# Optimization experiments

Hardware: AMD Instinct MI355X
Metric: run time of the kernel (lower is better)

The kernel has to match this reference:

```python
import jax, jax.numpy as jnp
import numpy as np

N_CELLS = 50000
N_GENES = 2000
HIDDEN = 128
HEADS = 4
HEAD_DIM = HIDDEN // HEADS
E_FULL = 800000
E_PRUNED = 400000
LN_EPS = 1e-6
NEG_SLOPE = 0.2


def setup_inputs() -> dict:
    key = jax.random.key(0)
    ks = jax.random.split(key, 20)
    s_in = 1.0 / np.sqrt(N_GENES)
    s_h = 1.0 / np.sqrt(HIDDEN)
    inp = {
        "node_features": jax.random.normal(ks[0], (N_CELLS, N_GENES), jnp.float32),
        "full_edge_index": jax.random.randint(ks[1], (2, E_FULL), 0, N_CELLS, jnp.int64 if jax.config.jax_enable_x64 else jnp.int32),
        "full_edge_weights": jax.random.uniform(ks[2], (E_FULL, 1), jnp.float32),
        "pruned_edge_index": jax.random.randint(ks[3], (2, E_PRUNED), 0, N_CELLS, jnp.int64 if jax.config.jax_enable_x64 else jnp.int32),
        "pruned_edge_weights": jax.random.uniform(ks[4], (E_PRUNED, 1), jnp.float32),
        "alpha": jax.random.uniform(ks[5], (), jnp.float32),
        # input projection
        "ip_w": jax.random.normal(ks[6], (N_GENES, HIDDEN), jnp.float32) * s_in,
        "ip_b": jnp.zeros((HIDDEN,), jnp.float32),
        # GAT full graph
        "gf_wsrc": jax.random.normal(ks[7], (HIDDEN, HIDDEN), jnp.float32) * s_h,
        "gf_wdst": jax.random.normal(ks[8], (HIDDEN, HIDDEN), jnp.float32) * s_h,
        "gf_wedge": jax.random.normal(ks[9], (1, HIDDEN), jnp.float32),
        "gf_attn": jax.random.normal(ks[10], (HEADS, HEAD_DIM), jnp.float32) * (1.0 / np.sqrt(HEAD_DIM)),
        "gf_bias": jnp.zeros((HIDDEN,), jnp.float32),
        # GAT pruned graph
        "gp_wsrc": jax.random.normal(ks[11], (HIDDEN, HIDDEN), jnp.float32) * s_h,
        "gp_wdst": jax.random.normal(ks[12], (HIDDEN, HIDDEN), jnp.float32) * s_h,
        "gp_wedge": jax.random.normal(ks[13], (1, HIDDEN), jnp.float32),
        "gp_attn": jax.random.normal(ks[14], (HEADS, HEAD_DIM), jnp.float32) * (1.0 / np.sqrt(HEAD_DIM)),
        "gp_bias": jnp.zeros((HIDDEN,), jnp.float32),
        # LayerNorm
        "ln_scale": jnp.ones((HIDDEN,), jnp.float32),
        "ln_bias": jnp.zeros((HIDDEN,), jnp.float32),
    }
    return inp


def _gatv2(h, edge_index, edge_w, wsrc, wdst, wedge, attn, bias):
    """GATv2 with edge features: e_ij = a_h . leaky_relu(Ws h_i + Wd h_j + We w_ij),
    segment-softmax over destination nodes, scatter-aggregate Ws h_src, concat heads."""
    n = h.shape[0]
    src, dst = edge_index[0], edge_index[1]
    hs = (h @ wsrc).reshape(n, HEADS, HEAD_DIM)
    hd = (h @ wdst).reshape(n, HEADS, HEAD_DIM)
    ew = (edge_w @ wedge).reshape(-1, HEADS, HEAD_DIM)  # [E,H,D]
    z = jax.nn.leaky_relu(hs[src] + hd[dst] + ew, NEG_SLOPE)  # [E,H,D]
    logits = jnp.einsum('ehd,hd->eh', z, attn)  # [E,H]
    # segment softmax over incoming edges of each dst node
    m = jax.ops.segment_max(logits, dst, num_segments=n)
    m = jnp.where(jnp.isfinite(m), m, 0.0)
    ex = jnp.exp(logits - m[dst])
    denom = jax.ops.segment_sum(ex, dst, num_segments=n)
    att = ex / (denom[dst] + 1e-16)  # [E,H]
    out = jax.ops.segment_sum(att[..., None] * hs[src], dst, num_segments=n)  # [n,H,D]
    return out.reshape(n, HIDDEN) + bias


def _layer_norm(x, scale, bias):
    mu = jnp.mean(x, axis=-1, keepdims=True)
    var = jnp.mean(jnp.square(x - mu), axis=-1, keepdims=True)
    return (x - mu) * jax.lax.rsqrt(var + LN_EPS) * scale + bias


def reference(node_features, full_edge_index, full_edge_weights, pruned_edge_index,
              pruned_edge_weights, alpha, ip_w, ip_b,
              gf_wsrc, gf_wdst, gf_wedge, gf_attn, gf_bias,
              gp_wsrc, gp_wdst, gp_wedge, gp_attn, gp_bias,
              ln_scale, ln_bias):
    h = node_features @ ip_w + ip_b  # [n, hidden]
    h_full = _gatv2(h, full_edge_index, full_edge_weights, gf_wsrc, gf_wdst, gf_wedge, gf_attn, gf_bias)
    h_pruned = _gatv2(h, pruned_edge_index, pruned_edge_weights, gp_wsrc, gp_wdst, gp_wedge, gp_attn, gp_bias)
    h = (1.0 - alpha) * h_full + alpha * h_pruned
    h = jax.nn.elu(h)
    return _layer_norm(h, ln_scale, ln_bias)
```

## Files before the change

### kernel.cpp

```cpp
#include <hip/hip_runtime.h>
#include <hip/hip_bf16.h>

#define N_GENES 2000
#define SA 72
#define SH 136

typedef __attribute__((ext_vector_type(8))) short frag8;
typedef __attribute__((ext_vector_type(4))) float facc4;

static __device__ __forceinline__ unsigned short f2bf(float f) {
    unsigned int u = __float_as_uint(f);
    unsigned int r = (u + 0x7FFFu + ((u >> 16) & 1u)) >> 16;
    return (unsigned short)r;
}
static __device__ __forceinline__ ushort2 pk2(float a, float b) {
    __hip_bfloat162 r = __float22bfloat162_rn(float2{a, b});
    return *(ushort2*)&r;
}

__global__ void prep(const float* __restrict__ ip_w,
                     const float* __restrict__ ws_f, const float* __restrict__ wd_f,
                     const float* __restrict__ ws_p, const float* __restrict__ wd_p,
                     unsigned short* __restrict__ Bt1,
                     unsigned short* __restrict__ Bf, unsigned short* __restrict__ Bp,
                     int* __restrict__ deg, unsigned int* __restrict__ counter, int n2) {
    int idx = blockIdx.x * blockDim.x + threadIdx.x;
    if (idx < n2) deg[idx] = 0;
    if (idx == 0) counter[0] = 0u;
    if (idx < 128 * 2048) {
        int nrow = idx >> 11, k = idx & 2047;
        unsigned short v = 0;
        if (k < N_GENES) v = f2bf(ip_w[(size_t)k * 128 + nrow]);
        Bt1[idx] = v;
    } else {
        int q = idx - 128 * 2048;
        if (q >= 2 * 256 * 128) return;
        int g = q >> 15;
        int r = (q >> 7) & 255;
        int k = q & 127;
        const float* w = (g == 0) ? (r < 128 ? ws_f : wd_f) : (r < 128 ? ws_p : wd_p);
        (g == 0 ? Bf : Bp)[(r << 7) | k] = f2bf(w[k * 128 + (r & 127)]);
    }
}

__global__ __launch_bounds__(256) void gemm_deg(const float* __restrict__ A,
                                                const unsigned short* __restrict__ Bt,
                                                const float* __restrict__ bias,
                                                const unsigned short* __restrict__ Bf,
                                                const unsigned short* __restrict__ Bp,
                                                unsigned short* __restrict__ Cf,
                                                unsigned short* __restrict__ Cp,
                                                int M, int K, int gemmBlocks,
                                                const int* __restrict__ dst_f, int Ef,
                                                const int* __restrict__ dst_p, int Ep,
                                                int* __restrict__ deg, int N) {
    if (blockIdx.x >= gemmBlocks) {
        int e = (blockIdx.x - gemmBlocks) * 256 + threadIdx.x;
        if (e < Ef) atomicAdd(&deg[dst_f[e]], 1);
        else if (e < Ef + Ep) atomicAdd(&deg[N + dst_p[e - Ef]], 1);
        return;
    }
    const int Kpad = 2048;
    __shared__ __align__(16) unsigned short lA[64 * SA];
    __shared__ __align__(16) unsigned short lH[64 * SH];
    int t = threadIdx.x, lane = t & 63, wv = t >> 6;
    int lr = lane & 15, lq = lane >> 4;
    facc4 acc[4][2];
#pragma unroll
    for (int i = 0; i < 4; i++)
#pragma unroll
        for (int j = 0; j < 2; j++) acc[i][j] = (facc4){0.f, 0.f, 0.f, 0.f};
    int row_base = blockIdx.x * 64;

    int ar_r[4], ar_c[4];
    const float* ar_p[4];
#pragma unroll
    for (int j = 0; j < 4; j++) {
        int q = j * 256 + t;
        ar_r[j] = q >> 4;
        ar_c[j] = (q & 15) * 4;
        int rg = row_base + ar_r[j];
        if (rg >= M) rg = M - 1;
        ar_p[j] = A + (size_t)rg * K + ar_c[j];
    }
    const unsigned short* bp[4];
#pragma unroll
    for (int ks = 0; ks < 2; ks++)
#pragma unroll
        for (int ni = 0; ni < 2; ni++) {
            int col = wv * 32 + ni * 16 + lr;
            bp[ks * 2 + ni] = Bt + (size_t)col * Kpad + ks * 32 + lq * 8;
        }

    float4 ar[4];
    frag8 bfr[4];
#pragma unroll
    for (int j = 0; j < 4; j++) ar[j] = *(const float4*)(ar_p[j]);
#pragma unroll
    for (int f = 0; f < 4; f++) bfr[f] = *(const frag8*)(bp[f]);

    for (int k0 = 0; k0 < Kpad; k0 += 64) {
        __syncthreads();
#pragma unroll
        for (int j = 0; j < 4; j++) {
            ushort2 u01 = pk2(ar[j].x, ar[j].y);
            ushort2 u23 = pk2(ar[j].z, ar[j].w);
            ushort4 u = {u01.x, u01.y, u23.x, u23.y};
            *(ushort4*)&lA[ar_r[j] * SA + ar_c[j]] = u;
        }
        __syncthreads();
        int kn = k0 + 64;
        frag8 bfn[4];
        if (kn < Kpad) {
#pragma unroll
            for (int j = 0; j < 4; j++) {
                int kk = kn + ar_c[j];
                float4 v = {0.f, 0.f, 0.f, 0.f};
                if (kk < K) v = *(const float4*)(ar_p[j] + kn);
                ar[j] = v;
            }
#pragma unroll
            for (int f = 0; f < 4; f++) bfn[f] = *(const frag8*)(bp[f] + kn);
        }
#pragma unroll
        for (int ks = 0; ks < 2; ks++) {
            frag8 af[4];
#pragma unroll
            for (int mi = 0; mi < 4; mi++)
                af[mi] = *(const frag8*)&lA[(mi * 16 + lr) * SA + ks * 32 + lq * 8];
#pragma unroll
            for (int mi = 0; mi < 4; mi++)
#pragma unroll
                for (int ni = 0; ni < 2; ni++)
                    acc[mi][ni] = __builtin_amdgcn_mfma_f32_16x16x32_bf16(af[mi], bfr[ks * 2 + ni], acc[mi][ni], 0, 0, 0);
        }
        if (kn < Kpad) {
#pragma unroll
            for (int f = 0; f < 4; f++) bfr[f] = bfn[f];
        }
    }
    __syncthreads();
#pragma unroll
    for (int mi = 0; mi < 4; mi++) {
#pragma unroll
        for (int r = 0; r < 4; r++) {
            int row = mi * 16 + lq * 4 + r;
#pragma unroll
            for (int ni = 0; ni < 2; ni++) {
                int col = wv * 32 + ni * 16 + lr;
                lH[row * SH + col] = f2bf(acc[mi][ni][r] + bias[col]);
            }
        }
    }
    __syncthreads();
#pragma unroll 1
    for (int g = 0; g < 2; g++) {
        const unsigned short* B2 = g ? Bp : Bf;
        unsigned short* Cb = g ? Cp : Cf;
        facc4 a2[4][4];
#pragma unroll
        for (int i = 0; i < 4; i++)
#pragma unroll
            for (int j = 0; j < 4; j++) a2[i][j] = (facc4){0.f, 0.f, 0.f, 0.f};
#pragma unroll
        for (int ks = 0; ks < 4; ks++) {
            frag8 af[4], bf[4];
#pragma unroll
            for (int mi = 0; mi < 4; mi++)
                af[mi] = *(const frag8*)&lH[(mi * 16 + lr) * SH + ks * 32 + lq * 8];
#pragma unroll
            for (int ni = 0; ni < 4; ni++)
                bf[ni] = *(const frag8*)(B2 + ((wv * 64 + ni * 16 + lr) << 7) + ks * 32 + lq * 8);
#pragma unroll
            for (int mi = 0; mi < 4; mi++)
#pragma unroll
                for (int ni = 0; ni < 4; ni++)
                    a2[mi][ni] = __builtin_amdgcn_mfma_f32_16x16x32_bf16(af[mi], bf[ni], a2[mi][ni], 0, 0, 0);
        }
#pragma unroll
        for (int mi = 0; mi < 4; mi++) {
#pragma unroll
            for (int r = 0; r < 4; r++) {
                int row = row_base + mi * 16 + lq * 4 + r;
                if (row < M) {
#pragma unroll
                    for (int ni = 0; ni < 4; ni++) {
                        int col = wv * 64 + ni * 16 + lr;
                        Cb[(size_t)row * 256 + col] = f2bf(a2[mi][ni][r]);
                    }
                }
            }
        }
    }
}

__global__ __launch_bounds__(256) void seg_assign(const int* __restrict__ deg,
                                                  int* __restrict__ offs,
                                                  int* __restrict__ cur,
                                                  unsigned int* __restrict__ counter, int n2) {
    int i = blockIdx.x * 256 + threadIdx.x;
    int lane = threadIdx.x & 63;
    int c = (i < n2) ? deg[i] : 0;
    int incl = c;
#pragma unroll
    for (int o = 1; o < 64; o <<= 1) {
        int y = __shfl_up(incl, o);
        if (lane >= o) incl += y;
    }
    int wtot = __shfl(incl, 63);
    int base = 0;
    if (lane == 63) base = (int)atomicAdd(counter, (unsigned int)wtot);
    base = __shfl(base, 63);
    int start = base + incl - c;
    if (i < n2) { offs[i] = start; cur[i] = start; }
}

__global__ void fill2(const int* __restrict__ src_f, const int* __restrict__ dst_f,
                      const float* __restrict__ ew_f, int Ef,
                      const int* __restrict__ src_p, const int* __restrict__ dst_p,
                      const float* __restrict__ ew_p, int Ep,
                      int* __restrict__ cur, int2* __restrict__ srcw, int N) {
    int e = blockIdx.x * blockDim.x + threadIdx.x;
    if (e >= Ef + Ep) return;
    int g = (e >= Ef);
    int ee = g ? e - Ef : e;
    int d = g ? dst_p[ee] : dst_f[ee];
    int node = g ? N + d : d;
    int p = atomicAdd(&cur[node], 1);
    int s = g ? src_p[ee] : src_f[ee];
    float w = g ? ew_p[ee] : ew_f[ee];
    srcw[p] = make_int2(s, __float_as_int(w));
}

static __device__ __forceinline__ float2 gat_node(const unsigned short* __restrict__ hshd,
                                                  const float* __restrict__ wedge,
                                                  const float* __restrict__ attn,
                                                  const float* __restrict__ bias,
                                                  const int2* __restrict__ srcw,
                                                  int s, int cnt, int onode, int d2) {
    const float LOG2E = 1.4426950408889634f;
    const float2 wv = *(const float2*)&wedge[d2];
    float2 av = *(const float2*)&attn[d2];
    av.x *= LOG2E; av.y *= LOG2E;
    unsigned int hdraw = *(const unsigned int*)&hshd[(size_t)onode * 256 + 128 + d2];
    const float hd0 = __uint_as_float(hdraw << 16);
    const float hd1 = __uint_as_float(hdraw & 0xffff0000u);
    float m = -INFINITY, l = 0.f, acc0 = 0.f, acc1 = 0.f;
    if (cnt > 0) {
        int last = s + cnt - 1;
        auto CL = [last](int j) { return j > last ? last : j; };
        int2 e0 = srcw[s], e1 = srcw[CL(s + 1)], e2 = srcw[CL(s + 2)], e3 = srcw[CL(s + 3)];
        int2 e4 = srcw[CL(s + 4)], e5 = srcw[CL(s + 5)];
        unsigned int hr0 = *(const unsigned int*)&hshd[(size_t)e0.x * 256 + d2];
        unsigned int hr1 = *(const unsigned int*)&hshd[(size_t)e1.x * 256 + d2];
        unsigned int hr2 = *(const unsigned int*)&hshd[(size_t)e2.x * 256 + d2];
        unsigned int hr3 = *(const unsigned int*)&hshd[(size_t)e3.x * 256 + d2];
        for (int i = 0; i < cnt; i += 2) {
            int2 ea = srcw[CL(s + i + 6)], eb = srcw[CL(s + i + 7)];
            unsigned int hr4 = *(const unsigned int*)&hshd[(size_t)e4.x * 256 + d2];
            unsigned int hr5 = *(const unsigned int*)&hshd[(size_t)e5.x * 256 + d2];
            {
                float h0 = __uint_as_float(hr0 << 16);
                float h1 = __uint_as_float(hr0 & 0xffff0000u);
                float w = __int_as_float(e0.y);
                float z0 = fmaf(w, wv.x, h0 + hd0); z0 = (z0 > 0.f) ? z0 : 0.2f * z0;
                float z1 = fmaf(w, wv.y, h1 + hd1); z1 = (z1 > 0.f) ? z1 : 0.2f * z1;
                float t = z0 * av.x + z1 * av.y;
                t += __shfl_xor(t, 1);
                t += __shfl_xor(t, 2);
                t += __shfl_xor(t, 4);
                t += __shfl_xor(t, 8);
                float mn = fmaxf(m, t);
                float sc = __builtin_amdgcn_exp2f(m - mn);
                float p = __builtin_amdgcn_exp2f(t - mn);
                l = l * sc + p;
                acc0 = acc0 * sc + p * h0;
                acc1 = acc1 * sc + p * h1;
                m = mn;
            }
            if (i + 1 < cnt) {
                float h0 = __uint_as_float(hr1 << 16);
                float h1 = __uint_as_float(hr1 & 0xffff0000u);
                float w = __int_as_float(e1.y);
                float z0 = fmaf(w, wv.x, h0 + hd0); z0 = (z0 > 0.f) ? z0 : 0.2f * z0;
                float z1 = fmaf(w, wv.y, h1 + hd1); z1 = (z1 > 0.f) ? z1 : 0.2f * z1;
                float t = z0 * av.x + z1 * av.y;
                t += __shfl_xor(t, 1);
                t += __shfl_xor(t, 2);
                t += __shfl_xor(t, 4);
                t += __shfl_xor(t, 8);
                float mn = fmaxf(m, t);
                float sc = __builtin_amdgcn_exp2f(m - mn);
                float p = __builtin_amdgcn_exp2f(t - mn);
                l = l * sc + p;
                acc0 = acc0 * sc + p * h0;
                acc1 = acc1 * sc + p * h1;
                m = mn;
            }
            e0 = e2; e1 = e3; e2 = e4; e3 = e5; e4 = ea; e5 = eb;
            hr0 = hr2; hr1 = hr3; hr2 = hr4; hr3 = hr5;
        }
    }
    float inv = 1.f / (l + 1e-16f);
    const float2 bv = *(const float2*)&bias[d2];
    return float2{acc0 * inv + bv.x, acc1 * inv + bv.y};
}

__global__ __launch_bounds__(256) void gat_final(const int* __restrict__ offs,
                                                 const int* __restrict__ deg,
                                                 const int2* __restrict__ srcw,
                                                 const unsigned short* __restrict__ hshd_f,
                                                 const unsigned short* __restrict__ hshd_p,
                                                 const float* __restrict__ wedge_f,
                                                 const float* __restrict__ attn_f,
                                                 const float* __restrict__ bias_f,
                                                 const float* __restrict__ wedge_p,
                                                 const float* __restrict__ attn_p,
                                                 const float* __restrict__ bias_p,
                                                 const float* __restrict__ alpha_p,
                                                 const float* __restrict__ scale,
                                                 const float* __restrict__ beta,
                                                 float* __restrict__ out, int N) {
    int node = blockIdx.x * 4 + (threadIdx.x >> 6);
    if (node >= N) return;
    int lane = threadIdx.x & 63;
    int d2 = lane * 2;
    float2 f = gat_node(hshd_f, wedge_f, attn_f, bias_f, srcw,
                        offs[node], deg[node], node, d2);
    float2 p = gat_node(hshd_p, wedge_p, attn_p, bias_p, srcw,
                        offs[N + node], deg[N + node], node, d2);
    float a = *alpha_p;
    float x0 = (1.f - a) * f.x + a * p.x;
    float x1 = (1.f - a) * f.y + a * p.y;
    x0 = (x0 > 0.f) ? x0 : expm1f(x0);
    x1 = (x1 > 0.f) ? x1 : expm1f(x1);
    float sm = x0 + x1;
#pragma unroll
    for (int o = 32; o >= 1; o >>= 1) sm += __shfl_xor(sm, o);
    float mu = sm * (1.f / 128.f);
    float d0 = x0 - mu, d1 = x1 - mu;
    float v = d0 * d0 + d1 * d1;
#pragma unroll
    for (int o = 32; o >= 1; o >>= 1) v += __shfl_xor(v, o);
    float rstd = rsqrtf(v * (1.f / 128.f) + 1e-6f);
    const float2 sv = *(const float2*)&scale[d2];
    const float2 bv = *(const float2*)&beta[d2];
    float2 o2;
    o2.x = d0 * rstd * sv.x + bv.x;
    o2.y = d1 * rstd * sv.y + bv.y;
    *(float2*)&out[(size_t)node * 128 + d2] = o2;
}

extern "C" void kernel_launch(void* const* d_in, const int* in_sizes, int n_in,
                              void* d_out, int out_size, void* d_ws, size_t ws_size,
                              hipStream_t stream) {
    const float* nf = (const float*)d_in[0];
    const int* fei = (const int*)d_in[1];
    const float* few = (const float*)d_in[2];
    const int* pei = (const int*)d_in[3];
    const float* pew = (const float*)d_in[4];
    const float* alpha = (const float*)d_in[5];
    const float* ip_w = (const float*)d_in[6];
    const float* ip_b = (const float*)d_in[7];
    const float* gf_wsrc = (const float*)d_in[8];
    const float* gf_wdst = (const float*)d_in[9];
    const float* gf_wedge = (const float*)d_in[10];
    const float* gf_attn = (const float*)d_in[11];
    const float* gf_bias = (const float*)d_in[12];
    const float* gp_wsrc = (const float*)d_in[13];
    const float* gp_wdst = (const float*)d_in[14];
    const float* gp_wedge = (const float*)d_in[15];
    const float* gp_attn = (const float*)d_in[16];
    const float* gp_bias = (const float*)d_in[17];
    const float* ln_scale = (const float*)d_in[18];
    const float* ln_bias = (const float*)d_in[19];

    const int N = in_sizes[0] / N_GENES;
    const int Ef = in_sizes[1] / 2;
    const int Ep = in_sizes[3] / 2;
    const int Etot = Ef + Ep;
    const int n2 = 2 * N;

    char* base = (char*)d_ws;
    size_t off = 0;
    auto carve = [&](size_t bytes) -> char* {
        char* p = base + off;
        off = (off + bytes + 255) & ~(size_t)255;
        return p;
    };
    unsigned short* Bt1 = (unsigned short*)carve((size_t)128 * 2048 * 2);
    unsigned short* Bf = (unsigned short*)carve(256 * 128 * 2);
    unsigned short* Bp = (unsigned short*)carve(256 * 128 * 2);
    unsigned short* hshd_f = (unsigned short*)carve((size_t)N * 256 * 2);
    unsigned short* hshd_p = (unsigned short*)carve((size_t)N * 256 * 2);
    int* deg = (int*)carve((size_t)n2 * 4);
    int* offs = (int*)carve((size_t)n2 * 4);
    int* cur = (int*)carve((size_t)n2 * 4);
    unsigned int* counter = (unsigned int*)carve(4);
    int2* srcw = (int2*)carve((size_t)Etot * 8);
    float* out_f = (float*)d_out;

    const int* src_f = fei;
    const int* dst_f = fei + Ef;
    const int* src_p = pei;
    const int* dst_p = pei + Ep;

    prep<<<(128 * 2048 + 2 * 256 * 128 + 255) / 256, 256, 0, stream>>>(
        ip_w, gf_wsrc, gf_wdst, gp_wsrc, gp_wdst, Bt1, Bf, Bp, deg, counter, n2);

    int gb1 = (N + 63) / 64;
    int degb = (Etot + 255) / 256;
    gemm_deg<<<gb1 + degb, 256, 0, stream>>>(nf, Bt1, ip_b, Bf, Bp, hshd_f, hshd_p,
                                             N, N_GENES, gb1,
                                             dst_f, Ef, dst_p, Ep, deg, N);

    seg_assign<<<(n2 + 255) / 256, 256, 0, stream>>>(deg, offs, cur, counter, n2);

    fill2<<<(Etot + 255) / 256, 256, 0, stream>>>(src_f, dst_f, few, Ef, src_p, dst_p, pew, Ep,
                                                  cur, srcw, N);

    gat_final<<<(N + 3) / 4, 256, 0, stream>>>(offs, deg, srcw, hshd_f, hshd_p,
                                               gf_wedge, gf_attn, gf_bias,
                                               gp_wedge, gp_attn, gp_bias,
                                               alpha, ln_scale, ln_bias, out_f, N);
    (void)ws_size; (void)n_in; (void)out_size;
}
```

Before: 830.9 us.

## Split fused dual-graph GAT kernel into per-graph wavefronts plus separate epilogue

The fused kernel that ran both GATv2 aggregations for a node in one wavefront is replaced by a kernel that gives each (graph, node) pair its own wavefront. The grid doubles, and each wavefront handles a single serial edge loop, which is meant to raise parallelism and latency hiding. Results go to an fp32 h_full scratch buffer and to the output buffer, and a second kernel then applies the alpha mix, ELU and LayerNorm. The cost is an extra launch and an extra write and read of two N×128 fp32 arrays.

Measured after the change: 823.7 us. Within noise of the previous version (-0.9%).

```diff
diff --git a/kernel.cpp b/kernel.cpp
--- a/kernel.cpp
+++ b/kernel.cpp
@@ -232,12 +232,30 @@
     srcw[p] = make_int2(s, __float_as_int(w));
 }
 
-static __device__ __forceinline__ float2 gat_node(const unsigned short* __restrict__ hshd,
-                                                  const float* __restrict__ wedge,
-                                                  const float* __restrict__ attn,
-                                                  const float* __restrict__ bias,
-                                                  const int2* __restrict__ srcw,
-                                                  int s, int cnt, int onode, int d2) {
+__global__ __launch_bounds__(256) void gat2(const int* __restrict__ offs,
+                                            const int* __restrict__ deg,
+                                            const int2* __restrict__ srcw,
+                                            const unsigned short* __restrict__ hshd_f,
+                                            const unsigned short* __restrict__ hshd_p,
+                                            const float* __restrict__ wedge_f,
+                                            const float* __restrict__ attn_f,
+                                            const float* __restrict__ bias_f,
+                                            const float* __restrict__ wedge_p,
+                                            const float* __restrict__ attn_p,
+                                            const float* __restrict__ bias_p,
+                                            float* __restrict__ out_full,
+                                            float* __restrict__ out_pruned, int N) {
+    int node = blockIdx.x * 4 + (threadIdx.x >> 6);
+    if (node >= 2 * N) return;
+    int g = node >= N;
+    int onode = g ? node - N : node;
+    const unsigned short* hshd = g ? hshd_p : hshd_f;
+    const float* wedge = g ? wedge_p : wedge_f;
+    const float* attn = g ? attn_p : attn_f;
+    const float* bias = g ? bias_p : bias_f;
+    float* out = g ? out_pruned : out_full;
+    int lane = threadIdx.x & 63;
+    int d2 = lane * 2;
     const float LOG2E = 1.4426950408889634f;
     const float2 wv = *(const float2*)&wedge[d2];
     float2 av = *(const float2*)&attn[d2];
@@ -245,6 +263,7 @@
     unsigned int hdraw = *(const unsigned int*)&hshd[(size_t)onode * 256 + 128 + d2];
     const float hd0 = __uint_as_float(hdraw << 16);
     const float hd1 = __uint_as_float(hdraw & 0xffff0000u);
+    int s = offs[node], cnt = deg[node];
     float m = -INFINITY, l = 0.f, acc0 = 0.f, acc1 = 0.f;
     if (cnt > 0) {
         int last = s + cnt - 1;
@@ -303,33 +322,24 @@
     }
     float inv = 1.f / (l + 1e-16f);
     const float2 bv = *(const float2*)&bias[d2];
-    return float2{acc0 * inv + bv.x, acc1 * inv + bv.y};
-}
-
-__global__ __launch_bounds__(256) void gat_final(const int* __restrict__ offs,
-                                                 const int* __restrict__ deg,
-                                                 const int2* __restrict__ srcw,
-                                                 const unsigned short* __restrict__ hshd_f,
-                                                 const unsigned short* __restrict__ hshd_p,
-                                                 const float* __restrict__ wedge_f,
-                                                 const float* __restrict__ attn_f,
-                                                 const float* __restrict__ bias_f,
-                                                 const float* __restrict__ wedge_p,
-                                                 const float* __restrict__ attn_p,
-                                                 const float* __restrict__ bias_p,
-                                                 const float* __restrict__ alpha_p,
-                                                 const float* __restrict__ scale,
-                                                 const float* __restrict__ beta,
-                                                 float* __restrict__ out, int N) {
+    float2 o;
+    o.x = acc0 * inv + bv.x;
+    o.y = acc1 * inv + bv.y;
+    *(float2*)&out[(size_t)onode * 128 + d2] = o;
+}
+
+__global__ __launch_bounds__(256) void final_kernel(const float* __restrict__ hf,
+                                                    float* __restrict__ out,
+                                                    const float* __restrict__ alpha_p,
+                                                    const float* __restrict__ scale,
+                                                    const float* __restrict__ beta, int n) {
     int node = blockIdx.x * 4 + (threadIdx.x >> 6);
-    if (node >= N) return;
+    if (node >= n) return;
     int lane = threadIdx.x & 63;
     int d2 = lane * 2;
-    float2 f = gat_node(hshd_f, wedge_f, attn_f, bias_f, srcw,
-                        offs[node], deg[node], node, d2);
-    float2 p = gat_node(hshd_p, wedge_p, attn_p, bias_p, srcw,
-                        offs[N + node], deg[N + node], node, d2);
     float a = *alpha_p;
+    float2 f = *(const float2*)&hf[(size_t)node * 128 + d2];
+    float2 p = *(const float2*)&out[(size_t)node * 128 + d2];
     float x0 = (1.f - a) * f.x + a * p.x;
     float x1 = (1.f - a) * f.y + a * p.y;
     x0 = (x0 > 0.f) ? x0 : expm1f(x0);
@@ -393,6 +403,7 @@
     unsigned short* Bp = (unsigned short*)carve(256 * 128 * 2);
     unsigned short* hshd_f = (unsigned short*)carve((size_t)N * 256 * 2);
     unsigned short* hshd_p = (unsigned short*)carve((size_t)N * 256 * 2);
+    float* h_full = (float*)carve((size_t)N * 128 * 4);
     int* deg = (int*)carve((size_t)n2 * 4);
     int* offs = (int*)carve((size_t)n2 * 4);
     int* cur = (int*)carve((size_t)n2 * 4);
@@ -419,9 +430,11 @@
     fill2<<<(Etot + 255) / 256, 256, 0, stream>>>(src_f, dst_f, few, Ef, src_p, dst_p, pew, Ep,
                                                   cur, srcw, N);
 
-    gat_final<<<(N + 3) / 4, 256, 0, stream>>>(offs, deg, srcw, hshd_f, hshd_p,
-                                               gf_wedge, gf_attn, gf_bias,
-                                               gp_wedge, gp_attn, gp_bias,
-                                               alpha, ln_scale, ln_bias, out_f, N);
+    gat2<<<(n2 + 3) / 4, 256, 0, stream>>>(offs, deg, srcw, hshd_f, hshd_p,
+                                           gf_wedge, gf_attn, gf_bias,
+                                           gp_wedge, gp_attn, gp_bias,
+                                           h_full, out_f, N);
+
+    final_kernel<<<(N + 3) / 4, 256, 0, stream>>>(h_full, out_f, alpha, ln_scale, ln_bias, N);
     (void)ws_size; (void)n_in; (void)out_size;
 }
```
